# Performance work log

Hardware: AMD Instinct MI355X
Metric: run time of the kernel (lower is better)

The kernel has to match this reference:

```python
import jax, jax.numpy as jnp
import numpy as np
import jax.scipy.special as jsp

N_RESERVOIR = 8192
N_INPUT = 64
N_LAYERS = 3
INPUT_SCALE = 0.4
RES_SCALE = 0.9
BIAS_SCALE = 0.1
ALPHA = 1.0  # activation_fn_args = (1.0,)
N_HADAMARD = 1 << int(np.ceil(np.log2(N_INPUT + N_RESERVOIR)))  # 16384
N_PADDING = N_HADAMARD - N_RESERVOIR - N_INPUT
BATCH = 512


def fwht(x):
    """Fast Walsh-Hadamard transform along last axis. x: [B, n], n a power of 2."""
    B, n = x.shape
    h = 1
    while h < n:
        x = x.reshape(B, n // (2 * h), 2, h)
        a = x[:, :, 0, :]
        b = x[:, :, 1, :]
        x = jnp.concatenate([a + b, a - b], axis=-1).reshape(B, n)
        h *= 2
    return x


def leaky_erf(x, state, alpha):
    return (1.0 - alpha) * state + alpha * jsp.erf(x)


def setup_inputs() -> dict:
    key = jax.random.key(0)
    k1, k2, k3, k4 = jax.random.split(key, 4)
    state = jax.random.normal(k1, (BATCH, N_RESERVOIR), dtype=jnp.float32)
    inputs = jax.random.normal(k2, (BATCH, N_INPUT), dtype=jnp.float32)
    bias = BIAS_SCALE * jax.random.normal(k3, (N_RESERVOIR,), dtype=jnp.float32)
    # structured-transform diagonals: random Rademacher signs, one per layer
    diag = jnp.where(jax.random.uniform(k4, (N_LAYERS, N_HADAMARD)) < 0.5, -1.0, 1.0).astype(jnp.float32)
    return {"state": state, "inputs": inputs, "bias": bias, "diag": diag}


def reference(state, inputs, bias, diag):
    B = state.shape[0]
    pad = jnp.zeros((B, N_PADDING), dtype=state.dtype)
    X = jnp.concatenate([RES_SCALE * state, INPUT_SCALE * inputs, pad], axis=1)  # [B, N_HADAMARD]
    for l in range(N_LAYERS):
        X = fwht(X * diag[l])
    z = X[:, :N_RESERVOIR] / N_HADAMARD + bias
    return leaky_erf(z, state, ALPHA)
```

## Files before the change

kernel.cpp:

```cpp
#include <hip/hip_runtime.h>
#include <math.h>

#define NH    16384
#define NRES  8192
#define NINP  64
#define BATCH 512

__device__ __forceinline__ constexpr int gfold(int v) {
    return ((v >> 5) & 7) ^ ((v >> 8) & 7) ^ ((v >> 11) & 7);
}
__device__ __forceinline__ constexpr int physf(int v) {
    return v ^ (gfold(v) << 2);
}

template <int S>
__device__ __forceinline__ void stage64(float x[64]) {
#pragma unroll
    for (int i = 0; i < 64; ++i) {
        if (!(i & S)) {
            float a = x[i], b = x[i | S];
            x[i]     = a + b;
            x[i | S] = a - b;
        }
    }
}

#define WRX(Q, OFF) do { _Pragma("unroll") \
    for (int j = 0; j < 16; ++j) \
        lds4[(unsigned)((Q) ^ physf(OFF)) >> 2] = \
            make_float4(x[4*j+0], x[4*j+1], x[4*j+2], x[4*j+3]); } while (0)

#define RDX(Q, OFF) do { _Pragma("unroll") \
    for (int j = 0; j < 16; ++j) { \
        float4 v = lds4[(unsigned)((Q) ^ physf(OFF)) >> 2]; \
        x[4*j+0] = v.x; x[4*j+1] = v.y; x[4*j+2] = v.z; x[4*j+3] = v.w; } } while (0)

#define WAVE_SYNC() asm volatile("s_waitcnt lgkmcnt(0)" ::: "memory")


__global__ __launch_bounds__(256, 2) void st_kernel(
    const float* __restrict__ state, const float* __restrict__ inputs,
    const float* __restrict__ bias,  const float* __restrict__ diag,
    float* __restrict__ out)
{
    __shared__ float4 lds4[NH / 4];
    const int t = threadIdx.x;
    const int r = blockIdx.x;
    const int l = t & 63, w = t >> 6;

    const int bB = ((l & 15) << 2) | ((l >> 4) << 10) | (w << 12);
    const int bC = (l << 2) | (w << 8);

    float x[64];

    if (t < 128) {
        const float* srow = state + (size_t)r * NRES + t * 64;
        const float* d0   = diag + t * 64;
#pragma unroll
        for (int j = 0; j < 16; ++j) {
            float4 v = *(const float4*)(srow + 4 * j);
            float4 d = *(const float4*)(d0 + 4 * j);
            x[4*j+0] = 0.9f * v.x * d.x; x[4*j+1] = 0.9f * v.y * d.y;
            x[4*j+2] = 0.9f * v.z * d.z; x[4*j+3] = 0.9f * v.w * d.w;
        }
    } else if (t == 128) {
        const float* irow = inputs + r * NINP;
        const float* d0   = diag + 8192;
#pragma unroll
        for (int j = 0; j < 16; ++j) {
            float4 v = *(const float4*)(irow + 4 * j);
            float4 d = *(const float4*)(d0 + 4 * j);
            x[4*j+0] = 0.4f * v.x * d.x; x[4*j+1] = 0.4f * v.y * d.y;
            x[4*j+2] = 0.4f * v.z * d.z; x[4*j+3] = 0.4f * v.w * d.w;
        }
    } else {
#pragma unroll
        for (int e = 0; e < 64; ++e) x[e] = 0.f;
    }

    stage64<1>(x); stage64<2>(x); stage64<4>(x);
    stage64<8>(x); stage64<16>(x); stage64<32>(x);

    { const int Q = physf(t << 6); WRX(Q, (j << 2)); }
    WAVE_SYNC();
    { const int Q = physf(bB); RDX(Q, (j << 6)); }
    stage64<4>(x); stage64<8>(x); stage64<16>(x); stage64<32>(x);

    { const int Q = physf(bB); WRX(Q, (j << 6)); }
    __syncthreads();
    { const int Q = physf(bC); RDX(Q, (j << 10)); }

    float4 pf[16];
    {
        const float* d1 = diag + NH + bC;
#pragma unroll
        for (int j = 0; j < 16; ++j) pf[j] = *(const float4*)(d1 + (j << 10));
    }
    stage64<4>(x); stage64<8>(x); stage64<16>(x); stage64<32>(x);
#pragma unroll
    for (int j = 0; j < 16; ++j) {
        x[4*j+0] *= pf[j].x; x[4*j+1] *= pf[j].y;
        x[4*j+2] *= pf[j].z; x[4*j+3] *= pf[j].w;
    }
    stage64<1>(x); stage64<2>(x);
    stage64<4>(x); stage64<8>(x); stage64<16>(x); stage64<32>(x);

    { const int Q = physf(bC); WRX(Q, (j << 10)); }
    WAVE_SYNC();
    { const int Q = physf(((l & 3) << 6) | ((l >> 2) << 10) | (w << 8)); RDX(Q, (j << 2)); }
    stage64<4>(x); stage64<8>(x); stage64<16>(x); stage64<32>(x);

    { const int Q = physf(((l & 3) << 6) | ((l >> 2) << 10) | (w << 8)); WRX(Q, (j << 2)); }
    __syncthreads();
    { const int Q = physf(bB); RDX(Q, (j << 6)); }

    {
        const float* d2 = diag + 2 * NH + bB;
#pragma unroll
        for (int j = 0; j < 16; ++j) pf[j] = *(const float4*)(d2 + (j << 6));
    }
    stage64<4>(x); stage64<8>(x); stage64<16>(x); stage64<32>(x);
#pragma unroll
    for (int j = 0; j < 16; ++j) {
        x[4*j+0] *= pf[j].x; x[4*j+1] *= pf[j].y;
        x[4*j+2] *= pf[j].z; x[4*j+3] *= pf[j].w;
    }
    stage64<1>(x); stage64<2>(x);
    stage64<4>(x); stage64<8>(x); stage64<16>(x); stage64<32>(x);

    { const int Q = physf(bB); WRX(Q, (j << 6)); }
    WAVE_SYNC();
    { const int Q = physf(t << 6); RDX(Q, (j << 2)); }
    stage64<4>(x); stage64<8>(x); stage64<16>(x); stage64<32>(x);

    { const int Q = physf(t << 6); WRX(Q, (j << 2)); }
    __syncthreads();
    { const int Q = physf(bC); RDX(Q, (j << 10)); }

    float4 bv[8];
#pragma unroll
    for (int j = 0; j < 8; ++j) bv[j] = *(const float4*)(bias + bC + (j << 10));

    stage64<4>(x); stage64<8>(x); stage64<16>(x); stage64<32>(x);

    {
        float* orow = out + (size_t)r * NRES;
        const float inv = 1.0f / (float)NH;
#pragma unroll
        for (int j = 0; j < 8; ++j) {
            float4 o;
            o.x = erff(x[4*j+0] * inv + bv[j].x);
            o.y = erff(x[4*j+1] * inv + bv[j].y);
            o.z = erff(x[4*j+2] * inv + bv[j].z);
            o.w = erff(x[4*j+3] * inv + bv[j].w);
            *(float4*)(orow + bC + (j << 10)) = o;
        }
    }
}

extern "C" void kernel_launch(void* const* d_in, const int* in_sizes, int n_in,
                              void* d_out, int out_size, void* d_ws, size_t ws_size,
                              hipStream_t stream) {
    (void)in_sizes; (void)n_in; (void)out_size; (void)d_ws; (void)ws_size;
    const float* state  = (const float*)d_in[0];
    const float* inputs = (const float*)d_in[1];
    const float* bias   = (const float*)d_in[2];
    const float* diag   = (const float*)d_in[3];
    float* out = (float*)d_out;

    hipLaunchKernelGGL(st_kernel, dim3(BATCH), dim3(256), 0, stream,
                       state, inputs, bias, diag, out);
}
```

Baseline: 29.07 us.

## Replace intra-wave LDS transposes with DPP and permlane swap exchanges

Replaces the three wave-local LDS write/read transposes in the FWHT pipeline with register exchanges built from DPP quad permutes and v_permlane16/32_swap instructions. The thread-to-element index mappings (bA, bB, bC, bD) are redesigned so the cross-wave LDS transposes still line up with the new layout. The aim is to cut LDS traffic and lgkmcnt waits. In exchange it adds many VALU select and permute operations per exchange, plus extra __syncthreads barriers before the LDS writes that used to be wave-local.

Result: slower. 30.21 us (+3.9%).

```diff
diff --git a/kernel.cpp b/kernel.cpp
--- a/kernel.cpp
+++ b/kernel.cpp
@@ -25,17 +25,44 @@
     }
 }
 
-#define WRX(Q, OFF) do { _Pragma("unroll") \
+template <int CTRL>
+__device__ __forceinline__ float dppf(float v) {
+    return __builtin_bit_cast(float,
+        __builtin_amdgcn_update_dpp(0, __builtin_bit_cast(int, v), CTRL, 0xF, 0xF, true));
+}
+
+__device__ __forceinline__ void shuffle_exchange(float x[64], bool odd0, bool odd1) {
+#pragma unroll
+    for (int e = 0; e < 64; ++e) if (!(e & 4)) {
+        float A = x[e], B = x[e + 4];
+        float dA = dppf<0xB1>(A), dB = dppf<0xB1>(B);
+        x[e]     = odd0 ? dB : A;
+        x[e + 4] = odd0 ? B  : dA;
+    }
+#pragma unroll
+    for (int e = 0; e < 64; ++e) if (!(e & 8)) {
+        float A = x[e], B = x[e + 8];
+        float dA = dppf<0x4E>(A), dB = dppf<0x4E>(B);
+        x[e]     = odd1 ? dB : A;
+        x[e + 8] = odd1 ? B  : dA;
+    }
+#pragma unroll
+    for (int e = 0; e < 64; ++e) if (!(e & 16))
+        asm("v_permlane16_swap_b32 %0, %1" : "+v"(x[e]), "+v"(x[e + 16]));
+#pragma unroll
+    for (int e = 0; e < 64; ++e) if (!(e & 32))
+        asm("v_permlane32_swap_b32 %0, %1" : "+v"(x[e]), "+v"(x[e + 32]));
+}
+
+#define WRX(Q, SH) do { _Pragma("unroll") \
     for (int j = 0; j < 16; ++j) \
-        lds4[(unsigned)((Q) ^ physf(OFF)) >> 2] = \
+        lds4[(unsigned)((Q) ^ physf(j << (SH))) >> 2] = \
             make_float4(x[4*j+0], x[4*j+1], x[4*j+2], x[4*j+3]); } while (0)
 
-#define RDX(Q, OFF) do { _Pragma("unroll") \
+#define RDX(Q, SH) do { _Pragma("unroll") \
     for (int j = 0; j < 16; ++j) { \
-        float4 v = lds4[(unsigned)((Q) ^ physf(OFF)) >> 2]; \
+        float4 v = lds4[(unsigned)((Q) ^ physf(j << (SH))) >> 2]; \
         x[4*j+0] = v.x; x[4*j+1] = v.y; x[4*j+2] = v.z; x[4*j+3] = v.w; } } while (0)
-
-#define WAVE_SYNC() asm volatile("s_waitcnt lgkmcnt(0)" ::: "memory")
 
 
 __global__ __launch_bounds__(256, 2) void st_kernel(
@@ -47,15 +74,19 @@
     const int t = threadIdx.x;
     const int r = blockIdx.x;
     const int l = t & 63, w = t >> 6;
-
-    const int bB = ((l & 15) << 2) | ((l >> 4) << 10) | (w << 12);
-    const int bC = (l << 2) | (w << 8);
+    const int l01 = l & 3, l23 = (l >> 2) & 3, l45 = (l >> 4) & 3;
+    const bool odd0 = (l & 1), odd1 = (l & 2);
+
+    const int bA = (w << 12) | (l23 << 10) | (l45 << 8) | (l01 << 6);
+    const int bB = (w << 12) | (l23 << 10) | (l45 << 4) | (l01 << 2);
+    const int bC = (w << 8)  | (l23 << 6)  | (l45 << 4) | (l01 << 2);
+    const int bD = (l45 << 12) | (l01 << 10) | (w << 8) | (l23 << 6);
 
     float x[64];
 
     if (t < 128) {
-        const float* srow = state + (size_t)r * NRES + t * 64;
-        const float* d0   = diag + t * 64;
+        const float* srow = state + (size_t)r * NRES + bA;
+        const float* d0   = diag + bA;
 #pragma unroll
         for (int j = 0; j < 16; ++j) {
             float4 v = *(const float4*)(srow + 4 * j);
@@ -65,7 +96,7 @@
         }
     } else if (t == 128) {
         const float* irow = inputs + r * NINP;
-        const float* d0   = diag + 8192;
+        const float* d0   = diag + NRES;
 #pragma unroll
         for (int j = 0; j < 16; ++j) {
             float4 v = *(const float4*)(irow + 4 * j);
@@ -81,14 +112,12 @@
     stage64<1>(x); stage64<2>(x); stage64<4>(x);
     stage64<8>(x); stage64<16>(x); stage64<32>(x);
 
-    { const int Q = physf(t << 6); WRX(Q, (j << 2)); }
-    WAVE_SYNC();
-    { const int Q = physf(bB); RDX(Q, (j << 6)); }
-    stage64<4>(x); stage64<8>(x); stage64<16>(x); stage64<32>(x);
-
-    { const int Q = physf(bB); WRX(Q, (j << 6)); }
-    __syncthreads();
-    { const int Q = physf(bC); RDX(Q, (j << 10)); }
+    shuffle_exchange(x, odd0, odd1);
+    stage64<4>(x); stage64<8>(x); stage64<16>(x); stage64<32>(x);
+
+    { const int Q = physf(bB); WRX(Q, 6); }
+    __syncthreads();
+    { const int Q = physf(bC); RDX(Q, 10); }
 
     float4 pf[16];
     {
@@ -105,14 +134,13 @@
     stage64<1>(x); stage64<2>(x);
     stage64<4>(x); stage64<8>(x); stage64<16>(x); stage64<32>(x);
 
-    { const int Q = physf(bC); WRX(Q, (j << 10)); }
-    WAVE_SYNC();
-    { const int Q = physf(((l & 3) << 6) | ((l >> 2) << 10) | (w << 8)); RDX(Q, (j << 2)); }
-    stage64<4>(x); stage64<8>(x); stage64<16>(x); stage64<32>(x);
-
-    { const int Q = physf(((l & 3) << 6) | ((l >> 2) << 10) | (w << 8)); WRX(Q, (j << 2)); }
-    __syncthreads();
-    { const int Q = physf(bB); RDX(Q, (j << 6)); }
+    shuffle_exchange(x, odd0, odd1);
+    stage64<4>(x); stage64<8>(x); stage64<16>(x); stage64<32>(x);
+
+    __syncthreads();
+    { const int Q = physf(bD); WRX(Q, 2); }
+    __syncthreads();
+    { const int Q = physf(bB); RDX(Q, 6); }
 
     {
         const float* d2 = diag + 2 * NH + bB;
@@ -128,14 +156,13 @@
     stage64<1>(x); stage64<2>(x);
     stage64<4>(x); stage64<8>(x); stage64<16>(x); stage64<32>(x);
 
-    { const int Q = physf(bB); WRX(Q, (j << 6)); }
-    WAVE_SYNC();
-    { const int Q = physf(t << 6); RDX(Q, (j << 2)); }
-    stage64<4>(x); stage64<8>(x); stage64<16>(x); stage64<32>(x);
-
-    { const int Q = physf(t << 6); WRX(Q, (j << 2)); }
-    __syncthreads();
-    { const int Q = physf(bC); RDX(Q, (j << 10)); }
+    shuffle_exchange(x, odd0, odd1);
+    stage64<4>(x); stage64<8>(x); stage64<16>(x); stage64<32>(x);
+
+    __syncthreads();
+    { const int Q = physf(bA); WRX(Q, 2); }
+    __syncthreads();
+    { const int Q = physf(bC); RDX(Q, 10); }
 
     float4 bv[8];
 #pragma unroll
```
